# Kernel tuning notes

Measured on AMD Instinct MI355X. Metric: run time of the kernel, lower is better.

The kernel has to match this reference:

```python
import jax, jax.numpy as jnp
import numpy as np

FIELD_DIMS = [100000, 1000, 100, 50]
NUM_FEATURES = 12
NUM_CAT = len(FIELD_DIMS)
NUM_CONT = NUM_FEATURES - NUM_CAT
D = 32            # embed_dim
HID = [64, 32]
B, T = 1024, 200
BN_EPS = 1e-5


def setup_inputs() -> dict:
    key = jax.random.key(0)
    ks = jax.random.split(key, 32)
    # x: [B, T, F]; first NUM_CAT cols are integer category ids stored as float
    cat_cols = [jax.random.randint(ks[i], (B, T, 1), 0, FIELD_DIMS[i]).astype(jnp.float32)
                for i in range(NUM_CAT)]
    cont_cols = jax.random.normal(ks[4], (B, T, NUM_CONT), dtype=jnp.float32)
    x = jnp.concatenate(cat_cols + [cont_cols], axis=-1)
    s = 0.05
    inp = {"x": x}
    for i, fd in enumerate(FIELD_DIMS):
        inp[f"emb{i}"] = jax.random.normal(ks[5 + i], (fd, D), dtype=jnp.float32) * s
        inp[f"lin{i}"] = jax.random.normal(ks[9 + i], (fd, D), dtype=jnp.float32) * s
    # Conv1d(1, D, 1) per continuous field == per-field affine map scalar -> D
    inp["cont_w"]  = jax.random.normal(ks[13], (NUM_CONT, D), dtype=jnp.float32) * s
    inp["cont_b"]  = jax.random.normal(ks[14], (NUM_CONT, D), dtype=jnp.float32) * s
    inp["clin_w"]  = jax.random.normal(ks[15], (NUM_CONT, D), dtype=jnp.float32) * s
    inp["clin_b"]  = jax.random.normal(ks[16], (NUM_CONT, D), dtype=jnp.float32) * s
    inp["fin_bias"] = jnp.zeros((D,), dtype=jnp.float32)
    # DNN tower: kernel_size-1 Conv1d == dense over channel dim
    dims = [NUM_FEATURES * D] + HID
    for li in range(len(HID)):
        fan_in = dims[li]
        inp[f"w{li+1}"] = jax.random.normal(ks[17 + 4 * li], (HID[li], fan_in), dtype=jnp.float32) / np.sqrt(fan_in)
        inp[f"b{li+1}"] = jnp.zeros((HID[li],), dtype=jnp.float32)
        inp[f"g{li+1}"] = jnp.ones((HID[li],), dtype=jnp.float32)
        inp[f"beta{li+1}"] = jnp.zeros((HID[li],), dtype=jnp.float32)
    inp["w_out"] = jax.random.normal(ks[30], (D, HID[-1]), dtype=jnp.float32) / np.sqrt(HID[-1])
    inp["b_out"] = jnp.zeros((D,), dtype=jnp.float32)
    return inp


def _batchnorm(h, g, b):
    # training-mode BN over (batch, time), biased variance (torch default)
    mu = h.mean(axis=(0, 1))
    var = h.var(axis=(0, 1))
    return g * (h - mu) * jax.lax.rsqrt(var + BN_EPS) + b


def reference(x, emb0, emb1, emb2, emb3, lin0, lin1, lin2, lin3,
              cont_w, cont_b, clin_w, clin_b, fin_bias,
              w1, b1, g1, beta1, w2, b2, g2, beta2, w_out, b_out):
    embs = [emb0, emb1, emb2, emb3]
    lins = [lin0, lin1, lin2, lin3]
    cat_idx = x[..., :NUM_CAT].astype(jnp.int32)          # [B,T,C]
    xc = x[..., NUM_CAT:]                                  # [B,T,Nc]

    # per-field embeddings -> [B,T,F,D]
    cat_emb = jnp.stack([embs[i][cat_idx[..., i]] for i in range(NUM_CAT)], axis=2)
    cont_emb = xc[..., None] * cont_w + cont_b             # [B,T,Nc,D]
    emb_all = jnp.concatenate([cat_emb, cont_emb], axis=2)  # [B,T,F,D]

    # FM pairwise interaction (sum-of-squares trick)
    s = emb_all.sum(axis=2)                                # [B,T,D]
    interaction = 0.5 * (s * s - (emb_all * emb_all).sum(axis=2))

    # linear terms
    lin_cat = sum(lins[i][cat_idx[..., i]] for i in range(NUM_CAT))      # [B,T,D]
    lin_cont = (xc[..., None] * clin_w + clin_b).sum(axis=2)             # [B,T,D]
    linear = lin_cat + lin_cont + fin_bias

    # DNN tower (k=1 convs == dense over F*D channels); dropout omitted (eval)
    h = emb_all.reshape(B, T, NUM_FEATURES * D)
    h = jax.nn.relu(_batchnorm(h @ w1.T + b1, g1, beta1))
    h = jax.nn.relu(_batchnorm(h @ w2.T + b2, g2, beta2))
    dnn = h @ w_out.T + b_out                              # [B,T,D]

    return linear + interaction + dnn                      # [B,T,D]
```

## Files before the change

### kernel.cpp

```cpp
#include <hip/hip_runtime.h>
#include <hip/hip_bf16.h>

typedef __hip_bfloat16 bf16;

#define ROWS 204800
#define N_INV (1.0f / 204800.0f)

__device__ float g_stats[256];
__device__ bf16  g_E1_0b[100000 * 64];
__device__ float g_E1_1[1000 * 64];
__device__ float g_E1_2[100 * 64];
__device__ float g_E1_3[50 * 64];
__device__ float g_U[8 * 64];
__device__ float g_Vb[64];
__device__ bf16  g_h1p[ROWS * 64];
__device__ bf16  g_h2p[ROWS * 32];
__device__ bf16  g_fmp[ROWS * 32];

__device__ __forceinline__ int clampi(int v, int hi) {
    return v < 0 ? 0 : (v > hi ? hi : v);
}
__device__ __forceinline__ float rl_f(float v, int l) {
    return __uint_as_float((unsigned int)__builtin_amdgcn_readlane((int)__float_as_uint(v), l));
}
__device__ __forceinline__ float us2f(unsigned short u) {
    return __uint_as_float(((unsigned int)u) << 16);
}

__device__ __forceinline__ int swz8(int d) {
    return (d & ~7) | ((d & 7) ^ ((d >> 3) & 7));
}
__device__ __forceinline__ int swz4(int d) {
    return (d & ~3) | ((d & 3) ^ (((d >> 2) ^ (d >> 4)) & 3));
}

#define GLOAD16(gp, lp)                                                        \
    __builtin_amdgcn_global_load_lds(                                          \
        (const __attribute__((address_space(1))) unsigned int*)(gp),           \
        (__attribute__((address_space(3))) unsigned int*)(lp), 16, 0, 0)

__global__ __launch_bounds__(64) void precompute_kernel(
    const float* __restrict__ emb1, const float* __restrict__ emb2, const float* __restrict__ emb3,
    const float* __restrict__ cont_w, const float* __restrict__ cont_b,
    const float* __restrict__ w1, const float* __restrict__ b1)
{
    int b = blockIdx.x;
    int k = threadIdx.x;
    __shared__ float row[32];

    if (b < 1150) {
        const float* tab; float* out; int i, colOff;
        if (b < 1000)      { tab = emb1; out = g_E1_1; i = b;        colOff = 32; }
        else if (b < 1100) { tab = emb2; out = g_E1_2; i = b - 1000; colOff = 64; }
        else               { tab = emb3; out = g_E1_3; i = b - 1100; colOff = 96; }
        if (k < 32) row[k] = tab[i * 32 + k];
        __syncthreads();
        const float* wr = w1 + k * 384 + colOff;
        float acc = 0.f;
        #pragma unroll
        for (int d = 0; d < 32; ++d) acc = fmaf(row[d], wr[d], acc);
        out[i * 64 + k] = acc;
    } else {
        g_stats[k]       = 0.f;
        g_stats[k + 64]  = 0.f;
        g_stats[k + 128] = 0.f;
        g_stats[k + 192] = 0.f;

        float vb = b1[k];
        #pragma unroll
        for (int j = 0; j < 8; ++j) {
            const float* wr = w1 + k * 384 + (4 + j) * 32;
            float u = 0.f;
            #pragma unroll
            for (int d = 0; d < 32; ++d) {
                float w = wr[d];
                u  = fmaf(cont_w[j * 32 + d], w, u);
                vb = fmaf(cont_b[j * 32 + d], w, vb);
            }
            g_U[j * 64 + k] = u;
        }
        g_Vb[k] = vb;
    }
}

__global__ __launch_bounds__(256) void e10_kernel(
    const float* __restrict__ emb0, const float* __restrict__ w1)
{
    int lane = threadIdx.x & 63;
    int wv   = threadIdx.x >> 6;
    int h    = lane >> 5;

    float w1col[32];
    {
        const float4* wr = (const float4*)(w1 + lane * 384);
        #pragma unroll
        for (int q = 0; q < 8; ++q) {
            float4 v = wr[q];
            w1col[4*q+0] = v.x; w1col[4*q+1] = v.y;
            w1col[4*q+2] = v.z; w1col[4*q+3] = v.w;
        }
    }

    for (int i = blockIdx.x * 8 + wv * 2; i < 100000; i += gridDim.x * 8) {
        int iA = i, iB = i + 1;
        float e = emb0[(h ? iB : iA) * 32 + (lane & 31)];

        float a0 = 0.f, a1 = 0.f, a2 = 0.f, a3 = 0.f;
        float b0 = 0.f, b1v = 0.f, b2v = 0.f, b3 = 0.f;
        #pragma unroll
        for (int dd = 0; dd < 32; dd += 4) {
            a0  = fmaf(rl_f(e, dd + 0),      w1col[dd + 0], a0);
            a1  = fmaf(rl_f(e, dd + 1),      w1col[dd + 1], a1);
            a2  = fmaf(rl_f(e, dd + 2),      w1col[dd + 2], a2);
            a3  = fmaf(rl_f(e, dd + 3),      w1col[dd + 3], a3);
            b0  = fmaf(rl_f(e, 32 + dd + 0), w1col[dd + 0], b0);
            b1v = fmaf(rl_f(e, 32 + dd + 1), w1col[dd + 1], b1v);
            b2v = fmaf(rl_f(e, 32 + dd + 2), w1col[dd + 2], b2v);
            b3  = fmaf(rl_f(e, 32 + dd + 3), w1col[dd + 3], b3);
        }
        g_E1_0b[iA * 64 + lane] = __float2bfloat16((a0 + a1) + (a2 + a3));
        g_E1_0b[iB * 64 + lane] = __float2bfloat16((b0 + b1v) + (b2v + b3));
    }
}

__global__ __launch_bounds__(256, 4) void phase1_kernel(
    const float* __restrict__ x,
    const float* __restrict__ emb0, const float* __restrict__ lin0,
    const float* __restrict__ emb1, const float* __restrict__ lin1,
    const float* __restrict__ emb2, const float* __restrict__ lin2,
    const float* __restrict__ emb3, const float* __restrict__ lin3,
    const float* __restrict__ cont_w, const float* __restrict__ cont_b,
    const float* __restrict__ clin_w, const float* __restrict__ clin_b,
    const float* __restrict__ fin_bias)
{
    __shared__ float lsum[64], lsq[64];

    int tid  = threadIdx.x;
    int lane = tid & 63;
    int wv   = tid >> 6;
    int d    = lane & 31;
    bool lo  = lane < 32;

    if (tid < 64) { lsum[tid] = 0.f; lsq[tid] = 0.f; }
    __syncthreads();

    float uk[8];
    #pragma unroll
    for (int j = 0; j < 8; ++j) uk[j] = g_U[j * 64 + lane];
    float vbk = g_Vb[lane];

    float p1[8], p2[8], fb = 0.f;
    if (lo) {
        #pragma unroll
        for (int j = 0; j < 8; ++j) { p1[j] = cont_w[j * 32 + d]; p2[j] = cont_b[j * 32 + d]; }
    } else {
        #pragma unroll
        for (int j = 0; j < 8; ++j) { p1[j] = clin_w[j * 32 + d]; p2[j] = clin_b[j * 32 + d]; }
        fb = fin_bias[d];
    }

    const float* T0 = lo ? emb0 : lin0;
    const float* T1 = lo ? emb1 : lin1;
    const float* T2 = lo ? emb2 : lin2;
    const float* T3 = lo ? emb3 : lin3;

    int gw   = blockIdx.x * 4 + wv;
    int base = gw * 16;

    float xs[4];
    #pragma unroll
    for (int g = 0; g < 4; ++g)
        xs[g] = (lane < 48) ? x[(base + 4 * g) * 12 + lane] : 0.f;

    float ga[2][4], gb[2][4], gc[2][4], gd[2][4], t1[2][4], t2[2][4], t3[2][4];
    unsigned short e0u[2][4];

    auto issue = [&](int g, int s) {
        #pragma unroll
        for (int t = 0; t < 4; ++t) {
            int f  = t * 12;
            int i0 = clampi((int)rl_f(xs[g], f + 0), 99999);
            int i1 = clampi((int)rl_f(xs[g], f + 1), 999);
            int i2 = clampi((int)rl_f(xs[g], f + 2), 99);
            int i3 = clampi((int)rl_f(xs[g], f + 3), 49);
            ga[s][t]  = T0[i0 * 32 + d];
            gb[s][t]  = T1[i1 * 32 + d];
            gc[s][t]  = T2[i2 * 32 + d];
            gd[s][t]  = T3[i3 * 32 + d];
            e0u[s][t] = ((const unsigned short*)g_E1_0b)[i0 * 64 + lane];
            t1[s][t]  = g_E1_1[i1 * 64 + lane];
            t2[s][t]  = g_E1_2[i2 * 64 + lane];
            t3[s][t]  = g_E1_3[i3 * 64 + lane];
        }
    };

    issue(0, 0);

    float ss = 0.f, qq = 0.f;

    #pragma unroll
    for (int g = 0; g < 4; ++g) {
        int s = g & 1;
        if (g < 3) issue(g + 1, (g + 1) & 1);

        #pragma unroll
        for (int t = 0; t < 4; ++t) {
            int r  = base + 4 * g + t;
            int fo = t * 12 + 4;
            float xc[8];
            #pragma unroll
            for (int j = 0; j < 8; ++j) xc[j] = rl_f(xs[g], fo + j);

            float va = ga[s][t], vb = gb[s][t], vc = gc[s][t], vd = gd[s][t];

            float half_val;
            if (lo) {
                float s0 = va + vb, s1 = vc + vd;
                float q0 = fmaf(va, va, vb * vb);
                float q1 = fmaf(vc, vc, vd * vd);
                #pragma unroll
                for (int j = 0; j < 8; ++j) {
                    float ce = fmaf(xc[j], p1[j], p2[j]);
                    if (j & 1) { s1 += ce; q1 = fmaf(ce, ce, q1); }
                    else       { s0 += ce; q0 = fmaf(ce, ce, q0); }
                }
                float sfull = s0 + s1;
                half_val = 0.5f * (sfull * sfull - (q0 + q1));
            } else {
                float l0 = va + vb + fb, l1 = vc + vd;
                #pragma unroll
                for (int j = 0; j < 8; ++j) {
                    if (j & 1) l1 = fmaf(xc[j], p1[j], l1 + p2[j]);
                    else       l0 = fmaf(xc[j], p1[j], l0 + p2[j]);
                }
                half_val = l0 + l1;
            }
            float other = __shfl(half_val, lane | 32);
            if (lo) g_fmp[r * 32 + d] = __float2bfloat16(half_val + other);

            float h1 = ((vbk + us2f(e0u[s][t])) + (t1[s][t] + t2[s][t])) + t3[s][t];
            #pragma unroll
            for (int j = 0; j < 8; ++j) h1 = fmaf(xc[j], uk[j], h1);

            g_h1p[r * 64 + lane] = __float2bfloat16(h1);
            ss += h1;
            qq = fmaf(h1, h1, qq);
        }
    }

    atomicAdd(&lsum[lane], ss);
    atomicAdd(&lsq[lane], qq);
    __syncthreads();
    if (tid < 64) {
        atomicAdd(&g_stats[tid], lsum[tid]);
        atomicAdd(&g_stats[64 + tid], lsq[tid]);
    }
}

__global__ __launch_bounds__(256) void phase2_kernel(
    const float* __restrict__ w2, const float* __restrict__ b2,
    const float* __restrict__ g1, const float* __restrict__ beta1)
{
    __shared__ float sa[64], sc[64];
    __shared__ float ls[64];
    __shared__ uint4 hbuf[4][512];

    int tid  = threadIdx.x;
    int lane = tid & 63;
    int wv   = tid >> 6;
    size_t rowBase = (size_t)(blockIdx.x * 4 + wv) * 64;

    {
        const char* gsrc = (const char*)g_h1p + rowBase * 128;
        #pragma unroll
        for (int i = 0; i < 8; ++i) {
            int dlin = (i << 6) + lane;
            GLOAD16(gsrc + swz8(dlin) * 16, &hbuf[wv][i << 6]);
        }
    }

    if (tid < 64) {
        float mu  = g_stats[tid] * N_INV;
        float var = g_stats[64 + tid] * N_INV - mu * mu;
        float a   = g1[tid] * rsqrtf(var + 1e-5f);
        sa[tid] = a;
        sc[tid] = beta1[tid] - a * mu;
        ls[tid] = 0.f;
    }
    __syncthreads();
    asm volatile("s_waitcnt vmcnt(0)" ::: "memory");

    const uint4* lrow = hbuf[wv] + (lane << 3);
    int r7 = lane & 7;

    float acc[32];
    #pragma unroll
    for (int m = 0; m < 32; ++m) acc[m] = 0.f;

    #pragma unroll
    for (int half = 0; half < 2; ++half) {
        uint4 u[4];
        #pragma unroll
        for (int q = 0; q < 4; ++q) u[q] = lrow[(half * 4 + q) ^ r7];

        float y[32];
        #pragma unroll
        for (int q = 0; q < 4; ++q) {
            unsigned int w4[4] = {u[q].x, u[q].y, u[q].z, u[q].w};
            #pragma unroll
            for (int j = 0; j < 4; ++j) {
                int i  = q * 4 + j;
                int ch = half * 32 + 2 * i;
                float f0 = __uint_as_float(w4[j] << 16);
                float f1 = __uint_as_float(w4[j] & 0xffff0000u);
                y[2*i]     = fmaxf(0.f, fmaf(sa[ch],     f0, sc[ch]));
                y[2*i + 1] = fmaxf(0.f, fmaf(sa[ch + 1], f1, sc[ch + 1]));
            }
        }

        #pragma unroll
        for (int m = 0; m < 32; ++m) {
            const float* wr = w2 + m * 64 + half * 32;
            float a0 = 0.f, a1 = 0.f, a2 = 0.f, a3 = 0.f;
            #pragma unroll
            for (int k = 0; k < 32; k += 4) {
                a0 = fmaf(y[k + 0], wr[k + 0], a0);
                a1 = fmaf(y[k + 1], wr[k + 1], a1);
                a2 = fmaf(y[k + 2], wr[k + 2], a2);
                a3 = fmaf(y[k + 3], wr[k + 3], a3);
            }
            acc[m] += (a0 + a1) + (a2 + a3);
        }
    }

    #pragma unroll
    for (int m = 0; m < 32; ++m) acc[m] += b2[m];

    uint4 o[4];
    unsigned int* ow = (unsigned int*)o;
    #pragma unroll
    for (int i = 0; i < 16; ++i) {
        unsigned int lo16 = (unsigned int)__bfloat16_as_ushort(__float2bfloat16(acc[2*i]));
        unsigned int hi16 = (unsigned int)__bfloat16_as_ushort(__float2bfloat16(acc[2*i + 1]));
        ow[i] = lo16 | (hi16 << 16);
    }

    #pragma unroll
    for (int q = 0; q < 4; ++q) hbuf[wv][swz4((lane << 2) + q)] = o[q];
    asm volatile("s_waitcnt lgkmcnt(0)" ::: "memory");
    {
        uint4* og = (uint4*)(g_h2p + rowBase * 32);
        #pragma unroll
        for (int i = 0; i < 4; ++i) {
            int dlin = (i << 6) + lane;
            og[dlin] = hbuf[wv][swz4(dlin)];
        }
    }

    #pragma unroll
    for (int c0 = 0; c0 < 32; c0 += 8) {
        float s[8], q[8];
        #pragma unroll
        for (int j = 0; j < 8; ++j) { s[j] = acc[c0 + j]; q[j] = s[j] * s[j]; }
        #pragma unroll
        for (int off = 32; off >= 1; off >>= 1) {
            #pragma unroll
            for (int j = 0; j < 8; ++j) {
                s[j] += __shfl_xor(s[j], off);
                q[j] += __shfl_xor(q[j], off);
            }
        }
        if (lane == 0) {
            #pragma unroll
            for (int j = 0; j < 8; ++j) {
                atomicAdd(&ls[c0 + j],      s[j]);
                atomicAdd(&ls[32 + c0 + j], q[j]);
            }
        }
    }
    __syncthreads();
    if (tid < 32)       atomicAdd(&g_stats[128 + tid], ls[tid]);
    else if (tid < 64)  atomicAdd(&g_stats[160 + (tid - 32)], ls[tid]);
}

__global__ __launch_bounds__(256) void phase3_kernel(
    const float* __restrict__ w_out, const float* __restrict__ b_out,
    const float* __restrict__ g2, const float* __restrict__ beta2,
    float* __restrict__ out)
{
    __shared__ float sa[32], sc[32];
    __shared__ uint4 sbuf[4][512];

    int tid  = threadIdx.x;
    int lane = tid & 63;
    int wv   = tid >> 6;
    size_t rowBase = (size_t)(blockIdx.x * 4 + wv) * 64;

    {
        const char* gh2 = (const char*)g_h2p + rowBase * 64;
        const char* gfm = (const char*)g_fmp + rowBase * 64;
        #pragma unroll
        for (int i = 0; i < 4; ++i) {
            int dlin = (i << 6) + lane;
            GLOAD16(gh2 + swz4(dlin) * 16, &sbuf[wv][i << 6]);
        }
        #pragma unroll
        for (int i = 0; i < 4; ++i) {
            int dlin = (i << 6) + lane;
            GLOAD16(gfm + swz4(dlin) * 16, &sbuf[wv][256 + (i << 6)]);
        }
    }

    if (tid < 32) {
        float mu  = g_stats[128 + tid] * N_INV;
        float var = g_stats[160 + tid] * N_INV - mu * mu;
        float a   = g2[tid] * rsqrtf(var + 1e-5f);
        sa[tid] = a;
        sc[tid] = beta2[tid] - a * mu;
    }
    __syncthreads();
    asm volatile("s_waitcnt vmcnt(0)" ::: "memory");

    uint4 u[4], fm4[4];
    #pragma unroll
    for (int q = 0; q < 4; ++q) {
        int gidx = swz4((lane << 2) + q);
        u[q]   = sbuf[wv][gidx];
        fm4[q] = sbuf[wv][256 + gidx];
    }

    float y2[32];
    #pragma unroll
    for (int q = 0; q < 4; ++q) {
        unsigned int w4[4] = {u[q].x, u[q].y, u[q].z, u[q].w};
        #pragma unroll
        for (int j = 0; j < 4; ++j) {
            int i = q * 4 + j;
            float f0 = __uint_as_float(w4[j] << 16);
            float f1 = __uint_as_float(w4[j] & 0xffff0000u);
            y2[2*i]     = fmaxf(0.f, fmaf(sa[2*i],     f0, sc[2*i]));
            y2[2*i + 1] = fmaxf(0.f, fmaf(sa[2*i + 1], f1, sc[2*i + 1]));
        }
    }

    float fmv[32];
    {
        const unsigned int* fw = (const unsigned int*)fm4;
        #pragma unroll
        for (int i = 0; i < 16; ++i) {
            fmv[2*i]     = __uint_as_float(fw[i] << 16);
            fmv[2*i + 1] = __uint_as_float(fw[i] & 0xffff0000u);
        }
    }

    float res[32];
    #pragma unroll
    for (int dd = 0; dd < 32; ++dd) {
        const float* wr = w_out + dd * 32;
        float a0 = fmv[dd] + b_out[dd], a1 = 0.f, a2 = 0.f, a3 = 0.f;
        #pragma unroll
        for (int k = 0; k < 32; k += 4) {
            a0 = fmaf(y2[k + 0], wr[k + 0], a0);
            a1 = fmaf(y2[k + 1], wr[k + 1], a1);
            a2 = fmaf(y2[k + 2], wr[k + 2], a2);
            a3 = fmaf(y2[k + 3], wr[k + 3], a3);
        }
        res[dd] = (a0 + a1) + (a2 + a3);
    }

    #pragma unroll
    for (int q = 0; q < 8; ++q) {
        uint4 v;
        v.x = __float_as_uint(res[4*q+0]);
        v.y = __float_as_uint(res[4*q+1]);
        v.z = __float_as_uint(res[4*q+2]);
        v.w = __float_as_uint(res[4*q+3]);
        sbuf[wv][swz8((lane << 3) + q)] = v;
    }
    asm volatile("s_waitcnt lgkmcnt(0)" ::: "memory");
    {
        uint4* og = (uint4*)(out + rowBase * 32);
        #pragma unroll
        for (int i = 0; i < 8; ++i) {
            int dlin = (i << 6) + lane;
            og[dlin] = sbuf[wv][swz8(dlin)];
        }
    }
}

extern "C" void kernel_launch(void* const* d_in, const int* in_sizes, int n_in,
                              void* d_out, int out_size, void* d_ws, size_t ws_size,
                              hipStream_t stream) {
    (void)in_sizes; (void)n_in; (void)out_size; (void)d_ws; (void)ws_size;

    const float* x       = (const float*)d_in[0];
    const float* emb0    = (const float*)d_in[1];
    const float* lin0    = (const float*)d_in[2];
    const float* emb1    = (const float*)d_in[3];
    const float* lin1    = (const float*)d_in[4];
    const float* emb2    = (const float*)d_in[5];
    const float* lin2    = (const float*)d_in[6];
    const float* emb3    = (const float*)d_in[7];
    const float* lin3    = (const float*)d_in[8];
    const float* cont_w  = (const float*)d_in[9];
    const float* cont_b  = (const float*)d_in[10];
    const float* clin_w  = (const float*)d_in[11];
    const float* clin_b  = (const float*)d_in[12];
    const float* fin_bias= (const float*)d_in[13];
    const float* w1      = (const float*)d_in[14];
    const float* b1      = (const float*)d_in[15];
    const float* g1      = (const float*)d_in[16];
    const float* beta1   = (const float*)d_in[17];
    const float* w2      = (const float*)d_in[18];
    const float* b2      = (const float*)d_in[19];
    const float* g2      = (const float*)d_in[20];
    const float* beta2   = (const float*)d_in[21];
    const float* w_out   = (const float*)d_in[22];
    const float* b_out   = (const float*)d_in[23];

    float* outp = (float*)d_out;

    hipLaunchKernelGGL(precompute_kernel, dim3(1151), dim3(64), 0, stream,
                       emb1, emb2, emb3, cont_w, cont_b, w1, b1);

    hipLaunchKernelGGL(e10_kernel, dim3(1600), dim3(256), 0, stream, emb0, w1);

    hipLaunchKernelGGL(phase1_kernel, dim3(3200), dim3(256), 0, stream,
                       x, emb0, lin0, emb1, lin1, emb2, lin2, emb3, lin3,
                       cont_w, cont_b, clin_w, clin_b, fin_bias);

    hipLaunchKernelGGL(phase2_kernel, dim3(800), dim3(256), 0, stream,
                       w2, b2, g1, beta1);

    hipLaunchKernelGGL(phase3_kernel, dim3(800), dim3(256), 0, stream,
                       w_out, b_out, g2, beta2, outp);
}
```

Before: 334.4 us.

## Fuse emb0 first-layer projection into phase1 and drop precomputed bf16 table

Removes the separate kernel that projected all 100000 emb0 rows through the first DNN layer into a bf16 table. Instead, phase1 keeps a 32-column slice of w1 in registers and computes the projection per row, broadcasting the gathered emb0 vector with readlane. This avoids writing a 12.8 MB intermediate and gathering from it, at the cost of redundant FMAs on 204800 rows and 32 extra registers per thread. The double-buffered gather prefetch is also replaced by a simple per-group load, which may reduce latency hiding.

```diff
diff --git a/kernel.cpp b/kernel.cpp
--- a/kernel.cpp
+++ b/kernel.cpp
@@ -7,7 +7,6 @@
 #define N_INV (1.0f / 204800.0f)
 
 __device__ float g_stats[256];
-__device__ bf16  g_E1_0b[100000 * 64];
 __device__ float g_E1_1[1000 * 64];
 __device__ float g_E1_2[100 * 64];
 __device__ float g_E1_3[50 * 64];
@@ -22,9 +21,6 @@
 }
 __device__ __forceinline__ float rl_f(float v, int l) {
     return __uint_as_float((unsigned int)__builtin_amdgcn_readlane((int)__float_as_uint(v), l));
-}
-__device__ __forceinline__ float us2f(unsigned short u) {
-    return __uint_as_float(((unsigned int)u) << 16);
 }
 
 __device__ __forceinline__ int swz8(int d) {
@@ -83,46 +79,6 @@
     }
 }
 
-__global__ __launch_bounds__(256) void e10_kernel(
-    const float* __restrict__ emb0, const float* __restrict__ w1)
-{
-    int lane = threadIdx.x & 63;
-    int wv   = threadIdx.x >> 6;
-    int h    = lane >> 5;
-
-    float w1col[32];
-    {
-        const float4* wr = (const float4*)(w1 + lane * 384);
-        #pragma unroll
-        for (int q = 0; q < 8; ++q) {
-            float4 v = wr[q];
-            w1col[4*q+0] = v.x; w1col[4*q+1] = v.y;
-            w1col[4*q+2] = v.z; w1col[4*q+3] = v.w;
-        }
-    }
-
-    for (int i = blockIdx.x * 8 + wv * 2; i < 100000; i += gridDim.x * 8) {
-        int iA = i, iB = i + 1;
-        float e = emb0[(h ? iB : iA) * 32 + (lane & 31)];
-
-        float a0 = 0.f, a1 = 0.f, a2 = 0.f, a3 = 0.f;
-        float b0 = 0.f, b1v = 0.f, b2v = 0.f, b3 = 0.f;
-        #pragma unroll
-        for (int dd = 0; dd < 32; dd += 4) {
-            a0  = fmaf(rl_f(e, dd + 0),      w1col[dd + 0], a0);
-            a1  = fmaf(rl_f(e, dd + 1),      w1col[dd + 1], a1);
-            a2  = fmaf(rl_f(e, dd + 2),      w1col[dd + 2], a2);
-            a3  = fmaf(rl_f(e, dd + 3),      w1col[dd + 3], a3);
-            b0  = fmaf(rl_f(e, 32 + dd + 0), w1col[dd + 0], b0);
-            b1v = fmaf(rl_f(e, 32 + dd + 1), w1col[dd + 1], b1v);
-            b2v = fmaf(rl_f(e, 32 + dd + 2), w1col[dd + 2], b2v);
-            b3  = fmaf(rl_f(e, 32 + dd + 3), w1col[dd + 3], b3);
-        }
-        g_E1_0b[iA * 64 + lane] = __float2bfloat16((a0 + a1) + (a2 + a3));
-        g_E1_0b[iB * 64 + lane] = __float2bfloat16((b0 + b1v) + (b2v + b3));
-    }
-}
-
 __global__ __launch_bounds__(256, 4) void phase1_kernel(
     const float* __restrict__ x,
     const float* __restrict__ emb0, const float* __restrict__ lin0,
@@ -131,7 +87,8 @@
     const float* __restrict__ emb3, const float* __restrict__ lin3,
     const float* __restrict__ cont_w, const float* __restrict__ cont_b,
     const float* __restrict__ clin_w, const float* __restrict__ clin_b,
-    const float* __restrict__ fin_bias)
+    const float* __restrict__ fin_bias,
+    const float* __restrict__ w1)
 {
     __shared__ float lsum[64], lsq[64];
 
@@ -144,6 +101,17 @@
     if (tid < 64) { lsum[tid] = 0.f; lsq[tid] = 0.f; }
     __syncthreads();
 
+    float w1c[32];
+    {
+        const float4* wrv = (const float4*)(w1 + lane * 384);
+        #pragma unroll
+        for (int q = 0; q < 8; ++q) {
+            float4 v = wrv[q];
+            w1c[4*q+0] = v.x; w1c[4*q+1] = v.y;
+            w1c[4*q+2] = v.z; w1c[4*q+3] = v.w;
+        }
+    }
+
     float uk[8];
     #pragma unroll
     for (int j = 0; j < 8; ++j) uk[j] = g_U[j * 64 + lane];
@@ -172,10 +140,11 @@
     for (int g = 0; g < 4; ++g)
         xs[g] = (lane < 48) ? x[(base + 4 * g) * 12 + lane] : 0.f;
 
-    float ga[2][4], gb[2][4], gc[2][4], gd[2][4], t1[2][4], t2[2][4], t3[2][4];
-    unsigned short e0u[2][4];
-
-    auto issue = [&](int g, int s) {
+    float ss = 0.f, qq = 0.f;
+
+    #pragma unroll
+    for (int g = 0; g < 4; ++g) {
+        float ga[4], gb[4], gc[4], gd[4], t1[4], t2[4], t3[4];
         #pragma unroll
         for (int t = 0; t < 4; ++t) {
             int f  = t * 12;
@@ -183,25 +152,14 @@
             int i1 = clampi((int)rl_f(xs[g], f + 1), 999);
             int i2 = clampi((int)rl_f(xs[g], f + 2), 99);
             int i3 = clampi((int)rl_f(xs[g], f + 3), 49);
-            ga[s][t]  = T0[i0 * 32 + d];
-            gb[s][t]  = T1[i1 * 32 + d];
-            gc[s][t]  = T2[i2 * 32 + d];
-            gd[s][t]  = T3[i3 * 32 + d];
-            e0u[s][t] = ((const unsigned short*)g_E1_0b)[i0 * 64 + lane];
-            t1[s][t]  = g_E1_1[i1 * 64 + lane];
-            t2[s][t]  = g_E1_2[i2 * 64 + lane];
-            t3[s][t]  = g_E1_3[i3 * 64 + lane];
-        }
-    };
-
-    issue(0, 0);
-
-    float ss = 0.f, qq = 0.f;
-
-    #pragma unroll
-    for (int g = 0; g < 4; ++g) {
-        int s = g & 1;
-        if (g < 3) issue(g + 1, (g + 1) & 1);
+            ga[t] = T0[i0 * 32 + d];
+            gb[t] = T1[i1 * 32 + d];
+            gc[t] = T2[i2 * 32 + d];
+            gd[t] = T3[i3 * 32 + d];
+            t1[t] = g_E1_1[i1 * 64 + lane];
+            t2[t] = g_E1_2[i2 * 64 + lane];
+            t3[t] = g_E1_3[i3 * 64 + lane];
+        }
 
         #pragma unroll
         for (int t = 0; t < 4; ++t) {
@@ -211,7 +169,17 @@
             #pragma unroll
             for (int j = 0; j < 8; ++j) xc[j] = rl_f(xs[g], fo + j);
 
-            float va = ga[s][t], vb = gb[s][t], vc = gc[s][t], vd = gd[s][t];
+            float va = ga[t], vb = gb[t], vc = gc[t], vd = gd[t];
+
+            float e0a = 0.f, e0b = 0.f, e0c = 0.f, e0d = 0.f;
+            #pragma unroll
+            for (int dd = 0; dd < 32; dd += 4) {
+                e0a = fmaf(rl_f(va, dd + 0), w1c[dd + 0], e0a);
+                e0b = fmaf(rl_f(va, dd + 1), w1c[dd + 1], e0b);
+                e0c = fmaf(rl_f(va, dd + 2), w1c[dd + 2], e0c);
+                e0d = fmaf(rl_f(va, dd + 3), w1c[dd + 3], e0d);
+            }
+            float e0f = (e0a + e0b) + (e0c + e0d);
 
             float half_val;
             if (lo) {
@@ -238,7 +206,7 @@
             float other = __shfl(half_val, lane | 32);
             if (lo) g_fmp[r * 32 + d] = __float2bfloat16(half_val + other);
 
-            float h1 = ((vbk + us2f(e0u[s][t])) + (t1[s][t] + t2[s][t])) + t3[s][t];
+            float h1 = ((vbk + e0f) + (t1[t] + t2[t])) + t3[t];
             #pragma unroll
             for (int j = 0; j < 8; ++j) h1 = fmaf(xc[j], uk[j], h1);
 
@@ -523,11 +491,9 @@
     hipLaunchKernelGGL(precompute_kernel, dim3(1151), dim3(64), 0, stream,
                        emb1, emb2, emb3, cont_w, cont_b, w1, b1);
 
-    hipLaunchKernelGGL(e10_kernel, dim3(1600), dim3(256), 0, stream, emb0, w1);
-
     hipLaunchKernelGGL(phase1_kernel, dim3(3200), dim3(256), 0, stream,
                        x, emb0, lin0, emb1, lin1, emb2, lin2, emb3, lin3,
-                       cont_w, cont_b, clin_w, clin_b, fin_bias);
+                       cont_w, cont_b, clin_w, clin_b, fin_bias, w1);
 
     hipLaunchKernelGGL(phase2_kernel, dim3(800), dim3(256), 0, stream,
                        w2, b2, g1, beta1);
```

Result: no change. 335.2 us (+0.3%).
